# Optimization experiments

Hardware: AMD Instinct MI355X
Metric: run time of the kernel (lower is better)

Reference implementation:

```python
import jax, jax.numpy as jnp
import numpy as np

B, HG, WG = 2, 64, 64
N = HG * WG
C_IN, C_HID, HEADS, C_OUT = 512, 256, 4, 512
NEG_SLOPE = 0.2   # PyG GATv2Conv default negative_slope
LN_EPS = 1e-5


def _grid_edges(h, w):
    """8-neighborhood grid graph, edge_index[0]=source, edge_index[1]=target."""
    nodes = np.arange(h * w).reshape(h, w)
    srcs, dsts = [], []
    for dh in (-1, 0, 1):
        for dw in (-1, 0, 1):
            if dh == 0 and dw == 0:
                continue
            r0, r1 = max(0, -dh), h - max(0, dh)
            c0, c1 = max(0, -dw), w - max(0, dw)
            srcs.append(nodes[r0:r1, c0:c1].ravel())
            dsts.append(nodes[r0 + dh:r1 + dh, c0 + dw:c1 + dw].ravel())
    return np.stack([np.concatenate(srcs), np.concatenate(dsts)]).astype(np.int64)


def setup_inputs() -> dict:
    key = jax.random.key(0)
    ks = iter(jax.random.split(key, 32))

    def p(shape, scale=0.02):
        return jax.random.normal(next(ks), shape, dtype=jnp.float32) * scale

    return {
        "rgb_features": jax.random.normal(next(ks), (B, N, C_IN), dtype=jnp.float32),
        "x_features": jax.random.normal(next(ks), (B, N, C_IN), dtype=jnp.float32),
        "edge_index": jnp.asarray(_grid_edges(HG, WG)),
        # modality_fusion: Linear(2*C_IN, C_HID) + LayerNorm
        "fusion_w": p((C_HID, 2 * C_IN)), "fusion_b": jnp.zeros((C_HID,), jnp.float32),
        "fusion_g": jnp.ones((C_HID,), jnp.float32), "fusion_beta": jnp.zeros((C_HID,), jnp.float32),
        # GATSegmentation.in_proj + norm
        "inproj_w": p((C_HID, C_HID)), "inproj_b": jnp.zeros((C_HID,), jnp.float32),
        "norm_g": jnp.ones((C_HID,), jnp.float32), "norm_b": jnp.zeros((C_HID,), jnp.float32),
        # GATv2Conv layer 0: C_HID -> C_HID, heads=4, concat=True
        "l0_wl": p((HEADS * C_HID, C_HID)), "l0_bl": jnp.zeros((HEADS * C_HID,), jnp.float32),
        "l0_wr": p((HEADS * C_HID, C_HID)), "l0_br": jnp.zeros((HEADS * C_HID,), jnp.float32),
        "l0_att": p((HEADS, C_HID)), "l0_bias": jnp.zeros((HEADS * C_HID,), jnp.float32),
        # GATv2Conv layer 1 (final): 4*C_HID -> C_HID, heads=1, concat=False
        "l1_wl": p((C_HID, HEADS * C_HID)), "l1_bl": jnp.zeros((C_HID,), jnp.float32),
        "l1_wr": p((C_HID, HEADS * C_HID)), "l1_br": jnp.zeros((C_HID,), jnp.float32),
        "l1_att": p((1, C_HID)), "l1_bias": jnp.zeros((C_HID,), jnp.float32),
        # final_proj: 1x1 conv C_HID -> C_OUT
        "fp_w": p((C_OUT, C_HID)), "fp_b": jnp.zeros((C_OUT,), jnp.float32),
    }


def _ln(x, g, b):
    mu = x.mean(-1, keepdims=True)
    v = ((x - mu) ** 2).mean(-1, keepdims=True)
    return (x - mu) * jax.lax.rsqrt(v + LN_EPS) * g + b


def _gatv2(x, src, dst, wl, bl, wr, br, att, bias, concat):
    """PyG GATv2Conv (share_weights=False): gather, leaky_relu logit, segment softmax over
    target neighborhoods, scatter-add aggregation."""
    n = x.shape[0]
    heads, c = att.shape
    xl = (x @ wl.T + bl).reshape(n, heads, c)   # source-side transform (x_j)
    xr = (x @ wr.T + br).reshape(n, heads, c)   # target-side transform (x_i)
    e = jax.nn.leaky_relu(xl[src] + xr[dst], NEG_SLOPE)        # [E, H, C]
    logit = jnp.einsum('ehc,hc->eh', e, att)                   # [E, H]
    m = jax.ops.segment_max(logit, dst, num_segments=n)
    p = jnp.exp(logit - m[dst])
    z = jax.ops.segment_sum(p, dst, num_segments=n)
    alpha = p / z[dst]                                          # softmax per target node
    out = jax.ops.segment_sum(xl[src] * alpha[..., None], dst, num_segments=n)  # [N, H, C]
    out = out.reshape(n, heads * c) if concat else out.mean(axis=1)
    return out + bias


def reference(rgb_features, x_features, edge_index, fusion_w, fusion_b, fusion_g, fusion_beta,
              inproj_w, inproj_b, norm_g, norm_b,
              l0_wl, l0_bl, l0_wr, l0_br, l0_att, l0_bias,
              l1_wl, l1_bl, l1_wr, l1_br, l1_att, l1_bias,
              fp_w, fp_b):
    b, n, _ = rgb_features.shape
    loops = jnp.arange(n, dtype=edge_index.dtype)  # PyG add_self_loops=True
    src = jnp.concatenate([edge_index[0], loops])
    dst = jnp.concatenate([edge_index[1], loops])

    def single(rgb, xm):  # one graph in the batch (original loops over B in Python)
        comb = jnp.concatenate([rgb, xm], axis=-1)                     # [N, 2*C_IN]
        f = jax.nn.relu(_ln(comb @ fusion_w.T + fusion_b, fusion_g, fusion_beta))
        h = jax.nn.relu(_ln(f @ inproj_w.T + inproj_b, norm_g, norm_b))
        h = jax.nn.relu(_gatv2(h, src, dst, l0_wl, l0_bl, l0_wr, l0_br, l0_att, l0_bias, True))
        h = jax.nn.relu(_gatv2(h, src, dst, l1_wl, l1_bl, l1_wr, l1_br, l1_att, l1_bias, False))
        return h                                                        # [N, C_HID]

    nodes = jax.vmap(single)(rgb_features, x_features)                  # [B, N, C_HID]
    img = nodes.reshape(b, HG, WG, C_HID)
    return jnp.einsum('bhwc,oc->bohw', img, fp_w) + fp_b[None, :, None, None]
```

## Files before the change

### kernel.cpp

```cpp
#include <hip/hip_runtime.h>


#define NNODE 4096
#define LN_EPS 1e-5f
#define LOG2E 1.4426950408889634f

typedef _Float16 half8 __attribute__((ext_vector_type(8)));
typedef _Float16 half4 __attribute__((ext_vector_type(4)));
typedef _Float16 h2 __attribute__((ext_vector_type(2)));
typedef float f32x4 __attribute__((ext_vector_type(4)));

__device__ __forceinline__ float wave_reduce_sum(float v) {
    #pragma unroll
    for (int off = 32; off > 0; off >>= 1) v += __shfl_xor(v, off, 64);
    return v;
}

__device__ __forceinline__ void gload_lds16(const void* g, void* l) {
    __builtin_amdgcn_global_load_lds(
        (const __attribute__((address_space(1))) void*)g,
        (__attribute__((address_space(3))) void*)l, 16, 0, 0);
}

template<int N> __device__ __forceinline__ void waitcnt_vm() {
    if constexpr (N <= 0)      asm volatile("s_waitcnt vmcnt(0)" ::: "memory");
    else if constexpr (N == 2) asm volatile("s_waitcnt vmcnt(2)" ::: "memory");
    else if constexpr (N == 3) asm volatile("s_waitcnt vmcnt(3)" ::: "memory");
    else if constexpr (N == 4) asm volatile("s_waitcnt vmcnt(4)" ::: "memory");
    else                       asm volatile("s_waitcnt vmcnt(8)" ::: "memory");
}
__device__ __forceinline__ void barrier_raw() {
    asm volatile("s_barrier" ::: "memory");
}

__device__ __forceinline__ int xcd_swz(int lin, int total) {
    return (lin & 7) * (total >> 3) + (lin >> 3);
}

template<int IT, int JT, int OUTMODE>
__global__ __launch_bounds__(256) void gemm3_k(
    const _Float16* __restrict__ A, const _Float16* __restrict__ W,
    const float* __restrict__ bias_lo, const float* __restrict__ bias_hi,
    int nsplit, void* __restrict__ Cout, int K, int N)
{
    constexpr int BM = 32 * IT, BN = 32 * JT;
    constexpr int CA = (BM * 4) / 256;
    constexpr int CB = (BN * 4) / 256;
    constexpr int L = CA + CB;
    __shared__ _Float16 ldsA[3][BM * 32];
    __shared__ _Float16 ldsB[3][BN * 32];

    const int tid = threadIdx.x;
    const int lin = blockIdx.y * gridDim.x + blockIdx.x;
    const int swz = xcd_swz(lin, gridDim.x * gridDim.y);
    const int m0 = (swz / gridDim.x) * BM, n0 = (swz % gridDim.x) * BN;
    const int lane = tid & 63, w = tid >> 6;
    const int fr = lane & 15, kq = lane >> 4;
    const int sq = (kq ^ (fr & 3)) * 8;
    const int wm = (w & 1) * (16 * IT), wn = (w >> 1) * (16 * JT);

    const _Float16* aP[CA]; int aC[CA];
    #pragma unroll
    for (int i = 0; i < CA; ++i) {
        const int c = i * 256 + tid, r = c >> 2, q = (c & 3) ^ (r & 3);
        aP[i] = A + (size_t)(m0 + r) * K + q * 8;
        aC[i] = c * 8;
    }
    const _Float16* bP[CB]; int bC[CB];
    #pragma unroll
    for (int i = 0; i < CB; ++i) {
        const int c = i * 256 + tid, r = c >> 2, q = (c & 3) ^ (r & 3);
        bP[i] = W + (size_t)(n0 + r) * K + q * 8;
        bC[i] = c * 8;
    }

    f32x4 acc[IT][JT] = {};
    const int NT = K >> 5;

    #pragma unroll
    for (int i = 0; i < CA; ++i) gload_lds16(aP[i], &ldsA[0][aC[i]]);
    #pragma unroll
    for (int i = 0; i < CB; ++i) gload_lds16(bP[i], &ldsB[0][bC[i]]);
    #pragma unroll
    for (int i = 0; i < CA; ++i) gload_lds16(aP[i] + 32, &ldsA[1][aC[i]]);
    #pragma unroll
    for (int i = 0; i < CB; ++i) gload_lds16(bP[i] + 32, &ldsB[1][bC[i]]);

    int bi = 0;
    for (int t = 0; t < NT; ++t) {
        if (t + 1 < NT) waitcnt_vm<L>(); else waitcnt_vm<0>();
        barrier_raw();
        if (t + 2 < NT) {
            int nb = bi + 2; if (nb >= 3) nb -= 3;
            const int k2 = (t + 2) << 5;
            #pragma unroll
            for (int i = 0; i < CA; ++i) gload_lds16(aP[i] + k2, &ldsA[nb][aC[i]]);
            #pragma unroll
            for (int i = 0; i < CB; ++i) gload_lds16(bP[i] + k2, &ldsB[nb][bC[i]]);
        }
        half8 af[IT], bf[JT];
        #pragma unroll
        for (int i = 0; i < IT; ++i)
            af[i] = *(const half8*)&ldsA[bi][(wm + i * 16 + fr) * 32 + sq];
        #pragma unroll
        for (int j = 0; j < JT; ++j)
            bf[j] = *(const half8*)&ldsB[bi][(wn + j * 16 + fr) * 32 + sq];
        #pragma unroll
        for (int i = 0; i < IT; ++i)
            #pragma unroll
            for (int j = 0; j < JT; ++j) {
                if (OUTMODE == 1)
                    acc[i][j] = __builtin_amdgcn_mfma_f32_16x16x32_f16(
                        bf[j], af[i], acc[i][j], 0, 0, 0);
                else
                    acc[i][j] = __builtin_amdgcn_mfma_f32_16x16x32_f16(
                        af[i], bf[j], acc[i][j], 0, 0, 0);
            }
        ++bi; if (bi == 3) bi = 0;
    }

    if (OUTMODE == 1) {
        #pragma unroll
        for (int i = 0; i < IT; ++i) {
            const int m = m0 + wm + i * 16 + fr;
            #pragma unroll
            for (int j = 0; j < JT; ++j) {
                const int nb4 = n0 + wn + j * 16 + kq * 4;
                const float* bp = (nb4 < nsplit) ? bias_lo + nb4
                                                 : bias_hi + (nb4 - nsplit);
                const float4 bv = *(const float4*)bp;
                half4 ov = {(_Float16)(acc[i][j][0] + bv.x),
                            (_Float16)(acc[i][j][1] + bv.y),
                            (_Float16)(acc[i][j][2] + bv.z),
                            (_Float16)(acc[i][j][3] + bv.w)};
                *(half4*)((_Float16*)Cout + (size_t)m * N + nb4) = ov;
            }
        }
    } else {
        #pragma unroll
        for (int j = 0; j < JT; ++j) {
            const int col = n0 + wn + j * 16 + fr;
            const float bc = (col < nsplit) ? bias_lo[col] : bias_hi[col - nsplit];
            #pragma unroll
            for (int i = 0; i < IT; ++i) {
                const int mrun = m0 + wm + i * 16 + kq * 4;
                const int b = mrun >> 12, node = mrun & 4095;
                float4 ov = {acc[i][j][0] + bc, acc[i][j][1] + bc,
                             acc[i][j][2] + bc, acc[i][j][3] + bc};
                *(float4*)((float*)Cout + ((size_t)(b * N + col)) * 4096 + node) = ov;
            }
        }
    }
}

__global__ __launch_bounds__(512) void fusion2_k(
    const float* __restrict__ A0, const float* __restrict__ A1,
    const _Float16* __restrict__ W1, const float* __restrict__ b1,
    const float* __restrict__ g1, const float* __restrict__ be1,
    const _Float16* __restrict__ W2, const float* __restrict__ b2,
    const float* __restrict__ g2, const float* __restrict__ be2,
    _Float16* __restrict__ out)
{
    __shared__ _Float16 lA[2][16 * 32];
    __shared__ _Float16 lB[2][256 * 32];
    __shared__ float lC[16 * 260];
    __shared__ _Float16 lH[8 * 512];

    const int tid = threadIdx.x;
    const int m0 = blockIdx.x * 16;
    const int lane = tid & 63, w = tid >> 6;
    const int fr = lane & 15, kq = lane >> 4;
    const int sq = (kq ^ (fr & 3)) * 8;
    const int wc = w * 32;
    const bool stager = (tid < 64);

    const _Float16* bP[2]; int bC[2];
    #pragma unroll
    for (int i = 0; i < 2; ++i) {
        const int c = i * 512 + tid, r = c >> 2, q = (c & 3) ^ (r & 3);
        bP[i] = W1 + (size_t)r * 1024 + q * 8;
        bC[i] = c * 8;
    }
    const int ar = tid >> 2, aq = tid & 3;
    const int asw = (ar * 4 + (aq ^ (ar & 3))) * 8;
    float4 p0, p1;
    auto loadA = [&](int k) {
        const int gk = k + aq * 8;
        const float* s = (gk < 512) ? A0 + (size_t)(m0 + ar) * 512 + gk
                                    : A1 + (size_t)(m0 + ar) * 512 + gk - 512;
        p0 = *(const float4*)s;
        p1 = *(const float4*)(s + 4);
    };
    auto writeA = [&](int b) {
        half8 hv = {(_Float16)p0.x, (_Float16)p0.y, (_Float16)p0.z, (_Float16)p0.w,
                    (_Float16)p1.x, (_Float16)p1.y, (_Float16)p1.z, (_Float16)p1.w};
        *(half8*)&lA[b][asw] = hv;
    };

    f32x4 acc[2] = {};

    if (stager) { loadA(0); writeA(0); }
    #pragma unroll
    for (int i = 0; i < 2; ++i) gload_lds16(bP[i], &lB[0][bC[i]]);
    asm volatile("s_waitcnt vmcnt(0)" ::: "memory");
    __syncthreads();

    int cur = 0;
    for (int t = 0; t < 32; ++t) {
        const int pf = (t + 1 < 32);
        if (pf) {
            const int k1 = (t + 1) << 5;
            if (stager) loadA(k1);
            #pragma unroll
            for (int i = 0; i < 2; ++i) gload_lds16(bP[i] + k1, &lB[cur ^ 1][bC[i]]);
        }
        const half8 af = *(const half8*)&lA[cur][fr * 32 + sq];
        half8 bf[2];
        #pragma unroll
        for (int j = 0; j < 2; ++j)
            bf[j] = *(const half8*)&lB[cur][(wc + j * 16 + fr) * 32 + sq];
        #pragma unroll
        for (int j = 0; j < 2; ++j)
            acc[j] = __builtin_amdgcn_mfma_f32_16x16x32_f16(af, bf[j], acc[j], 0, 0, 0);
        if (pf) {
            if (stager) writeA(cur ^ 1);
            asm volatile("s_waitcnt vmcnt(0)" ::: "memory");
            __syncthreads();
            cur ^= 1;
        }
    }

    #pragma unroll
    for (int j = 0; j < 2; ++j) {
        const int col = wc + j * 16 + fr;
        const float bc = b1[col];
        #pragma unroll
        for (int r4 = 0; r4 < 4; ++r4)
            lC[(kq * 4 + r4) * 260 + col] = acc[j][r4] + bc;
    }
    __syncthreads();

    {
        const float4 gv = *(const float4*)(g1 + lane * 4);
        const float4 bv = *(const float4*)(be1 + lane * 4);
        const int t2i = lane >> 3, gq = (lane >> 1) & 3, qo = (lane & 1) * 4;
        #pragma unroll
        for (int rr = 0; rr < 2; ++rr) {
            const int row = w * 2 + rr;
            const float4 v = *(const float4*)&lC[row * 260 + lane * 4];
            float s  = v.x + v.y + v.z + v.w;
            float s2 = v.x * v.x + v.y * v.y + v.z * v.z + v.w * v.w;
            s = wave_reduce_sum(s);
            s2 = wave_reduce_sum(s2);
            const float mu  = s * (1.0f / 256.0f);
            const float var = s2 * (1.0f / 256.0f) - mu * mu;
            const float rs  = rsqrtf(var + LN_EPS);
            half4 o;
            o[0] = (_Float16)fmaxf((v.x - mu) * rs * gv.x + bv.x, 0.f);
            o[1] = (_Float16)fmaxf((v.y - mu) * rs * gv.y + bv.y, 0.f);
            o[2] = (_Float16)fmaxf((v.z - mu) * rs * gv.z + bv.z, 0.f);
            o[3] = (_Float16)fmaxf((v.w - mu) * rs * gv.w + bv.w, 0.f);
            const int qslot = gq ^ (row & 3);
            *(half4*)&lH[t2i * 512 + (row * 4 + qslot) * 8 + qo] = o;
        }
    }
    __syncthreads();

    const _Float16* b2P[2]; int b2C[2];
    #pragma unroll
    for (int i = 0; i < 2; ++i) {
        const int c = i * 512 + tid, r = c >> 2, q = (c & 3) ^ (r & 3);
        b2P[i] = W2 + (size_t)r * 256 + q * 8;
        b2C[i] = c * 8;
    }
    f32x4 acc2[2] = {};
    #pragma unroll
    for (int i = 0; i < 2; ++i) gload_lds16(b2P[i], &lB[0][b2C[i]]);
    asm volatile("s_waitcnt vmcnt(0)" ::: "memory");
    __syncthreads();

    int cur2 = 0;
    for (int t2 = 0; t2 < 8; ++t2) {
        const int pf = (t2 + 1 < 8);
        if (pf) {
            const int k1 = (t2 + 1) << 5;
            #pragma unroll
            for (int i = 0; i < 2; ++i) gload_lds16(b2P[i] + k1, &lB[cur2 ^ 1][b2C[i]]);
        }
        const half8 af = *(const half8*)
            &lH[t2 * 512 + (fr * 4 + (kq ^ (fr & 3))) * 8];
        half8 bf[2];
        #pragma unroll
        for (int j = 0; j < 2; ++j)
            bf[j] = *(const half8*)&lB[cur2][(wc + j * 16 + fr) * 32 + sq];
        #pragma unroll
        for (int j = 0; j < 2; ++j)
            acc2[j] = __builtin_amdgcn_mfma_f32_16x16x32_f16(af, bf[j], acc2[j], 0, 0, 0);
        if (pf) {
            asm volatile("s_waitcnt vmcnt(0)" ::: "memory");
            __syncthreads();
            cur2 ^= 1;
        }
    }

    __syncthreads();
    #pragma unroll
    for (int j = 0; j < 2; ++j) {
        const int col = wc + j * 16 + fr;
        const float bc = b2[col];
        #pragma unroll
        for (int r4 = 0; r4 < 4; ++r4)
            lC[(kq * 4 + r4) * 260 + col] = acc2[j][r4] + bc;
    }
    __syncthreads();

    {
        const float4 gv = *(const float4*)(g2 + lane * 4);
        const float4 bv = *(const float4*)(be2 + lane * 4);
        #pragma unroll
        for (int rr = 0; rr < 2; ++rr) {
            const int row = w * 2 + rr;
            const float4 v = *(const float4*)&lC[row * 260 + lane * 4];
            float s  = v.x + v.y + v.z + v.w;
            float s2 = v.x * v.x + v.y * v.y + v.z * v.z + v.w * v.w;
            s = wave_reduce_sum(s);
            s2 = wave_reduce_sum(s2);
            const float mu  = s * (1.0f / 256.0f);
            const float var = s2 * (1.0f / 256.0f) - mu * mu;
            const float rs  = rsqrtf(var + LN_EPS);
            half4 o;
            o[0] = (_Float16)fmaxf((v.x - mu) * rs * gv.x + bv.x, 0.f);
            o[1] = (_Float16)fmaxf((v.y - mu) * rs * gv.y + bv.y, 0.f);
            o[2] = (_Float16)fmaxf((v.z - mu) * rs * gv.z + bv.z, 0.f);
            o[3] = (_Float16)fmaxf((v.w - mu) * rs * gv.w + bv.w, 0.f);
            *(half4*)(out + (size_t)(m0 + row) * 256 + lane * 4) = o;
        }
    }
}

template<int HEADS, int LD, int XROFF, int OC>
__global__ __launch_bounds__(256) void gat4_k(
    const _Float16* __restrict__ xlr, const _Float16* __restrict__ att16,
    const float* __restrict__ bias, _Float16* __restrict__ out)
{
    const int tid = threadIdx.x, wv = tid >> 6, lane = tid & 63;
    const int g = lane >> 4, li = lane & 15;
    const int blk = xcd_swz(blockIdx.x, gridDim.x);
    const int wid = blk * 4 + wv;
    const int gi = (HEADS == 4) ? wid : wid * 4 + g;
    const int h  = (HEADS == 4) ? g : 0;
    const int node = gi & (NNODE - 1);
    const int base = gi - node;
    const int nr = node >> 6, nc = node & 63;
    const int co = h * 256 + li * 16;

    int sidx[9]; float msk[9];
    {
        const int drs[8] = {-1,-1,-1, 0, 0, 1, 1, 1};
        const int dcs[8] = {-1, 0, 1,-1, 1,-1, 0, 1};
        #pragma unroll
        for (int j = 0; j < 8; ++j) {
            const int rj = nr + drs[j], cj = nc + dcs[j];
            const bool v = ((unsigned)rj < 64u) & ((unsigned)cj < 64u);
            sidx[j] = v ? (rj * 64 + cj) : node;
            msk[j] = v ? 0.f : -1e30f;
        }
        sidx[8] = node; msk[8] = 0.f;
    }

    const _Float16* xp = xlr + (size_t)base * LD + co;

    half8 x0[9], x1[9];
    #pragma unroll
    for (int j = 0; j < 9; ++j) {
        x0[j] = *(const half8*)(xp + (size_t)sidx[j] * LD);
        x1[j] = *(const half8*)(xp + (size_t)sidx[j] * LD + 8);
    }
    const half8 xr0 = *(const half8*)(xlr + (size_t)gi * LD + XROFF + co);
    const half8 xr1 = *(const half8*)(xlr + (size_t)gi * LD + XROFF + co + 8);
    const half8 at0 = *(const half8*)(att16 + h * 256 + li * 16);
    const half8 at1 = *(const half8*)(att16 + h * 256 + li * 16 + 8);
    const h2 hz = {(_Float16)0.f, (_Float16)0.f};
    const h2 c02 = {(_Float16)0.2f, (_Float16)0.2f};

    float lg[9];
    #pragma unroll
    for (int j = 0; j < 9; ++j) {
        h2 p = hz;
        #pragma unroll
        for (int k = 0; k < 4; ++k) {
            h2 e = ((const h2*)&x0[j])[k] + ((const h2*)&xr0)[k];
            h2 tt = __builtin_elementwise_fma(
                __builtin_elementwise_min(e, hz), c02,
                __builtin_elementwise_max(e, hz));
            p = __builtin_elementwise_fma(tt, ((const h2*)&at0)[k], p);
        }
        #pragma unroll
        for (int k = 0; k < 4; ++k) {
            h2 e = ((const h2*)&x1[j])[k] + ((const h2*)&xr1)[k];
            h2 tt = __builtin_elementwise_fma(
                __builtin_elementwise_min(e, hz), c02,
                __builtin_elementwise_max(e, hz));
            p = __builtin_elementwise_fma(tt, ((const h2*)&at1)[k], p);
        }
        float pl = (float)p[0] + (float)p[1];
        pl += __shfl_xor(pl, 1, 64);
        pl += __shfl_xor(pl, 2, 64);
        pl += __shfl_xor(pl, 4, 64);
        pl += __shfl_xor(pl, 8, 64);
        lg[j] = pl + msk[j];
    }

    float m = lg[0];
    #pragma unroll
    for (int j = 1; j < 9; ++j) m = fmaxf(m, lg[j]);
    float pj[9], z = 0.f;
    #pragma unroll
    for (int j = 0; j < 9; ++j) { pj[j] = __builtin_amdgcn_exp2f(lg[j] - m); z += pj[j]; }
    const float inv = __builtin_amdgcn_rcpf(z);

    float acc[16];
    #pragma unroll
    for (int k = 0; k < 16; ++k) acc[k] = 0.f;
    #pragma unroll
    for (int j = 0; j < 9; ++j) {
        const float wj = pj[j];
        #pragma unroll
        for (int k = 0; k < 8; ++k) acc[k]     += wj * (float)x0[j][k];
        #pragma unroll
        for (int k = 0; k < 8; ++k) acc[8 + k] += wj * (float)x1[j][k];
    }
    float bv[16];
    #pragma unroll
    for (int q = 0; q < 4; ++q) {
        const float4 b4 = *(const float4*)(bias + h * 256 + li * 16 + q * 4);
        bv[q * 4 + 0] = b4.x; bv[q * 4 + 1] = b4.y;
        bv[q * 4 + 2] = b4.z; bv[q * 4 + 3] = b4.w;
    }
    half8 o0, o1;
    #pragma unroll
    for (int k = 0; k < 8; ++k) o0[k] = (_Float16)fmaxf(acc[k] * inv + bv[k], 0.f);
    #pragma unroll
    for (int k = 0; k < 8; ++k) o1[k] = (_Float16)fmaxf(acc[8 + k] * inv + bv[8 + k], 0.f);
    *(half8*)(out + (size_t)gi * OC + co) = o0;
    *(half8*)(out + (size_t)gi * OC + co + 8) = o1;
}

struct WTab {
    const float* src[9];
    int startblk[10];
    int nelem[9];
    int dstoff[9];
    float scale[9];
};

__global__ __launch_bounds__(256) void wconv_k(WTab t, _Float16* __restrict__ dst)
{
    const int b = blockIdx.x;
    int s = 0;
    #pragma unroll
    for (int i = 1; i < 9; ++i) s += (b >= t.startblk[i]);
    const int e0 = (b - t.startblk[s]) * 1024 + threadIdx.x * 4;
    if (e0 >= t.nelem[s]) return;
    const float4 v = *(const float4*)(t.src[s] + e0);
    const float sc = t.scale[s];
    half4 o = {(_Float16)(v.x * sc), (_Float16)(v.y * sc),
               (_Float16)(v.z * sc), (_Float16)(v.w * sc)};
    *(half4*)(dst + t.dstoff[s] + e0) = o;
}

extern "C" void kernel_launch(void* const* d_in, const int* in_sizes, int n_in,
                              void* d_out, int out_size, void* d_ws, size_t ws_size,
                              hipStream_t stream)
{
    const float* rgb       = (const float*)d_in[0];
    const float* xm        = (const float*)d_in[1];
    const float* fusion_w  = (const float*)d_in[3];
    const float* fusion_b  = (const float*)d_in[4];
    const float* fusion_g  = (const float*)d_in[5];
    const float* fusion_be = (const float*)d_in[6];
    const float* inproj_w  = (const float*)d_in[7];
    const float* inproj_b  = (const float*)d_in[8];
    const float* norm_g    = (const float*)d_in[9];
    const float* norm_b    = (const float*)d_in[10];
    const float* l0_wl     = (const float*)d_in[11];
    const float* l0_bl     = (const float*)d_in[12];
    const float* l0_wr     = (const float*)d_in[13];
    const float* l0_br     = (const float*)d_in[14];
    const float* l0_att    = (const float*)d_in[15];
    const float* l0_bias   = (const float*)d_in[16];
    const float* l1_wl     = (const float*)d_in[17];
    const float* l1_bl     = (const float*)d_in[18];
    const float* l1_wr     = (const float*)d_in[19];
    const float* l1_br     = (const float*)d_in[20];
    const float* l1_att    = (const float*)d_in[21];
    const float* l1_bias   = (const float*)d_in[22];
    const float* fp_w      = (const float*)d_in[23];
    const float* fp_b      = (const float*)d_in[24];

    char* ws = (char*)d_ws;
    _Float16* Wf16 = (_Float16*)ws;
    _Float16* H1   = (_Float16*)(ws + 4194304);
    _Float16* XLR0 = (_Float16*)(ws + 8388608);
    _Float16* GO0  = (_Float16*)(ws + 41943040);
    _Float16* XLR1 = (_Float16*)(ws + 58720256);
    _Float16* GO1  = (_Float16*)(ws + 67108864);

    _Float16* w_fus  = Wf16 + 0;
    _Float16* w_inp  = Wf16 + 262144;
    _Float16* w_l0   = Wf16 + 327680;
    _Float16* w_l1   = Wf16 + 851968;
    _Float16* w_fp   = Wf16 + 1376256;
    _Float16* att0_h = Wf16 + 1507328;
    _Float16* att1_h = Wf16 + 1508352;

    WTab t;
    const float* srcs[9] = {fusion_w, inproj_w, l0_wl, l0_wr, l1_wl, l1_wr,
                            fp_w, l0_att, l1_att};
    const int nel[9]  = {262144, 65536, 262144, 262144, 262144, 262144,
                         131072, 1024, 256};
    const int doff[9] = {0, 262144, 327680, 589824, 851968, 1114112,
                         1376256, 1507328, 1508352};
    const int sblk[10] = {0, 256, 320, 576, 832, 1088, 1344, 1472, 1473, 1474};
    for (int i = 0; i < 9; ++i) {
        t.src[i] = srcs[i]; t.nelem[i] = nel[i]; t.dstoff[i] = doff[i];
        t.scale[i] = (i >= 7) ? LOG2E : 1.0f;
    }
    for (int i = 0; i < 10; ++i) t.startblk[i] = sblk[i];

    wconv_k<<<1474, 256, 0, stream>>>(t, Wf16);

    fusion2_k<<<512, 512, 0, stream>>>(
        rgb, xm, w_fus, fusion_b, fusion_g, fusion_be,
        w_inp, inproj_b, norm_g, norm_b, H1);

    gemm3_k<4, 4, 1><<<dim3(16, 64), 256, 0, stream>>>(
        H1, w_l0, l0_bl, l0_br, 1024, XLR0, 256, 2048);

    gat4_k<4, 2048, 1024, 1024><<<2048, 256, 0, stream>>>(
        XLR0, att0_h, l0_bias, GO0);

    gemm3_k<2, 4, 1><<<dim3(4, 128), 256, 0, stream>>>(
        GO0, w_l1, l1_bl, l1_br, 256, XLR1, 1024, 512);

    gat4_k<1, 512, 256, 256><<<512, 256, 0, stream>>>(
        XLR1, att1_h, l1_bias, GO1);

    gemm3_k<2, 4, 2><<<dim3(4, 128), 256, 0, stream>>>(
        GO1, w_fp, fp_b, fp_b, 512, d_out, 256, 512);
}
```

Before: 117.4 us.

## Pre-convert fusion inputs to fp16 and triple-buffer fusion GEMM loads

The fp32 rgb and x inputs are now converted to fp16 and concatenated in a prep kernel that also converts the weights, replacing the separate weight-conversion launch. The fusion kernel can then stream A through async global-to-LDS loads like B. Both GEMM loops move from double to triple buffering, using partial vmcnt waits and a single barrier per step instead of full drains. This adds a full extra write and read of the converted activation buffer and more LDS per block, in exchange for better overlap of loads with MFMA work.

```diff
diff --git a/kernel.cpp b/kernel.cpp
--- a/kernel.cpp
+++ b/kernel.cpp
@@ -153,16 +153,16 @@
     }
 }
 
-__global__ __launch_bounds__(512) void fusion2_k(
-    const float* __restrict__ A0, const float* __restrict__ A1,
+__global__ __launch_bounds__(512) void fusion3_k(
+    const _Float16* __restrict__ Af,
     const _Float16* __restrict__ W1, const float* __restrict__ b1,
     const float* __restrict__ g1, const float* __restrict__ be1,
     const _Float16* __restrict__ W2, const float* __restrict__ b2,
     const float* __restrict__ g2, const float* __restrict__ be2,
     _Float16* __restrict__ out)
 {
-    __shared__ _Float16 lA[2][16 * 32];
-    __shared__ _Float16 lB[2][256 * 32];
+    __shared__ _Float16 lA[3][16 * 32];
+    __shared__ _Float16 lB[3][256 * 32];
     __shared__ float lC[16 * 260];
     __shared__ _Float16 lH[8 * 512];
 
@@ -181,53 +181,40 @@
         bP[i] = W1 + (size_t)r * 1024 + q * 8;
         bC[i] = c * 8;
     }
-    const int ar = tid >> 2, aq = tid & 3;
-    const int asw = (ar * 4 + (aq ^ (ar & 3))) * 8;
-    float4 p0, p1;
-    auto loadA = [&](int k) {
-        const int gk = k + aq * 8;
-        const float* s = (gk < 512) ? A0 + (size_t)(m0 + ar) * 512 + gk
-                                    : A1 + (size_t)(m0 + ar) * 512 + gk - 512;
-        p0 = *(const float4*)s;
-        p1 = *(const float4*)(s + 4);
-    };
-    auto writeA = [&](int b) {
-        half8 hv = {(_Float16)p0.x, (_Float16)p0.y, (_Float16)p0.z, (_Float16)p0.w,
-                    (_Float16)p1.x, (_Float16)p1.y, (_Float16)p1.z, (_Float16)p1.w};
-        *(half8*)&lA[b][asw] = hv;
-    };
+    const int arow = tid >> 2, aq = (tid & 3) ^ (arow & 3);
+    const _Float16* aP = Af + (size_t)(m0 + arow) * 1024 + aq * 8;
+    const int aC = tid * 8;
 
     f32x4 acc[2] = {};
 
-    if (stager) { loadA(0); writeA(0); }
+    if (stager) gload_lds16(aP, &lA[0][aC]);
     #pragma unroll
     for (int i = 0; i < 2; ++i) gload_lds16(bP[i], &lB[0][bC[i]]);
-    asm volatile("s_waitcnt vmcnt(0)" ::: "memory");
-    __syncthreads();
-
-    int cur = 0;
+    if (stager) gload_lds16(aP + 32, &lA[1][aC]);
+    #pragma unroll
+    for (int i = 0; i < 2; ++i) gload_lds16(bP[i] + 32, &lB[1][bC[i]]);
+
+    int bi = 0;
     for (int t = 0; t < 32; ++t) {
-        const int pf = (t + 1 < 32);
-        if (pf) {
-            const int k1 = (t + 1) << 5;
-            if (stager) loadA(k1);
-            #pragma unroll
-            for (int i = 0; i < 2; ++i) gload_lds16(bP[i] + k1, &lB[cur ^ 1][bC[i]]);
-        }
-        const half8 af = *(const half8*)&lA[cur][fr * 32 + sq];
+        if (t + 1 < 32) { if (stager) waitcnt_vm<3>(); else waitcnt_vm<2>(); }
+        else            waitcnt_vm<0>();
+        barrier_raw();
+        if (t + 2 < 32) {
+            int nb = bi + 2; if (nb >= 3) nb -= 3;
+            const int k2 = (t + 2) << 5;
+            if (stager) gload_lds16(aP + k2, &lA[nb][aC]);
+            #pragma unroll
+            for (int i = 0; i < 2; ++i) gload_lds16(bP[i] + k2, &lB[nb][bC[i]]);
+        }
+        const half8 af = *(const half8*)&lA[bi][fr * 32 + sq];
         half8 bf[2];
         #pragma unroll
         for (int j = 0; j < 2; ++j)
-            bf[j] = *(const half8*)&lB[cur][(wc + j * 16 + fr) * 32 + sq];
+            bf[j] = *(const half8*)&lB[bi][(wc + j * 16 + fr) * 32 + sq];
         #pragma unroll
         for (int j = 0; j < 2; ++j)
             acc[j] = __builtin_amdgcn_mfma_f32_16x16x32_f16(af, bf[j], acc[j], 0, 0, 0);
-        if (pf) {
-            if (stager) writeA(cur ^ 1);
-            asm volatile("s_waitcnt vmcnt(0)" ::: "memory");
-            __syncthreads();
-            cur ^= 1;
-        }
+        ++bi; if (bi == 3) bi = 0;
     }
 
     #pragma unroll
@@ -276,31 +263,29 @@
     f32x4 acc2[2] = {};
     #pragma unroll
     for (int i = 0; i < 2; ++i) gload_lds16(b2P[i], &lB[0][b2C[i]]);
-    asm volatile("s_waitcnt vmcnt(0)" ::: "memory");
-    __syncthreads();
-
-    int cur2 = 0;
+    #pragma unroll
+    for (int i = 0; i < 2; ++i) gload_lds16(b2P[i] + 32, &lB[1][b2C[i]]);
+
+    int bi2 = 0;
     for (int t2 = 0; t2 < 8; ++t2) {
-        const int pf = (t2 + 1 < 8);
-        if (pf) {
-            const int k1 = (t2 + 1) << 5;
-            #pragma unroll
-            for (int i = 0; i < 2; ++i) gload_lds16(b2P[i] + k1, &lB[cur2 ^ 1][b2C[i]]);
+        if (t2 + 1 < 8) waitcnt_vm<2>(); else waitcnt_vm<0>();
+        barrier_raw();
+        if (t2 + 2 < 8) {
+            int nb = bi2 + 2; if (nb >= 3) nb -= 3;
+            const int k2 = (t2 + 2) << 5;
+            #pragma unroll
+            for (int i = 0; i < 2; ++i) gload_lds16(b2P[i] + k2, &lB[nb][b2C[i]]);
         }
         const half8 af = *(const half8*)
             &lH[t2 * 512 + (fr * 4 + (kq ^ (fr & 3))) * 8];
         half8 bf[2];
         #pragma unroll
         for (int j = 0; j < 2; ++j)
-            bf[j] = *(const half8*)&lB[cur2][(wc + j * 16 + fr) * 32 + sq];
+            bf[j] = *(const half8*)&lB[bi2][(wc + j * 16 + fr) * 32 + sq];
         #pragma unroll
         for (int j = 0; j < 2; ++j)
             acc2[j] = __builtin_amdgcn_mfma_f32_16x16x32_f16(af, bf[j], acc2[j], 0, 0, 0);
-        if (pf) {
-            asm volatile("s_waitcnt vmcnt(0)" ::: "memory");
-            __syncthreads();
-            cur2 ^= 1;
-        }
+        ++bi2; if (bi2 == 3) bi2 = 0;
     }
 
     __syncthreads();
@@ -454,9 +439,24 @@
     float scale[9];
 };
 
-__global__ __launch_bounds__(256) void wconv_k(WTab t, _Float16* __restrict__ dst)
+__global__ __launch_bounds__(256) void prep_k(
+    const float* __restrict__ rgb, const float* __restrict__ xm,
+    _Float16* __restrict__ Cf16, WTab t, _Float16* __restrict__ dst)
 {
-    const int b = blockIdx.x;
+    if (blockIdx.x < 4096) {
+        const int idx = blockIdx.x * 256 + threadIdx.x;
+        const int m = idx >> 7;
+        const int k = (idx & 127) * 8;
+        const float* s = (k < 512) ? rgb + (size_t)m * 512 + k
+                                   : xm  + (size_t)m * 512 + (k - 512);
+        const float4 v0 = *(const float4*)s;
+        const float4 v1 = *(const float4*)(s + 4);
+        half8 o = {(_Float16)v0.x, (_Float16)v0.y, (_Float16)v0.z, (_Float16)v0.w,
+                   (_Float16)v1.x, (_Float16)v1.y, (_Float16)v1.z, (_Float16)v1.w};
+        *(half8*)(Cf16 + (size_t)m * 1024 + k) = o;
+        return;
+    }
+    const int b = blockIdx.x - 4096;
     int s = 0;
     #pragma unroll
     for (int i = 1; i < 9; ++i) s += (b >= t.startblk[i]);
@@ -505,6 +505,7 @@
     _Float16* GO0  = (_Float16*)(ws + 41943040);
     _Float16* XLR1 = (_Float16*)(ws + 58720256);
     _Float16* GO1  = (_Float16*)(ws + 67108864);
+    _Float16* Cf16 = (_Float16*)(ws + 71303168);
 
     _Float16* w_fus  = Wf16 + 0;
     _Float16* w_inp  = Wf16 + 262144;
@@ -528,10 +529,10 @@
     }
     for (int i = 0; i < 10; ++i) t.startblk[i] = sblk[i];
 
-    wconv_k<<<1474, 256, 0, stream>>>(t, Wf16);
-
-    fusion2_k<<<512, 512, 0, stream>>>(
-        rgb, xm, w_fus, fusion_b, fusion_g, fusion_be,
+    prep_k<<<4096 + 1474, 256, 0, stream>>>(rgb, xm, Cf16, t, Wf16);
+
+    fusion3_k<<<512, 512, 0, stream>>>(
+        Cf16, w_fus, fusion_b, fusion_g, fusion_be,
         w_inp, inproj_b, norm_g, norm_b, H1);
 
     gemm3_k<4, 4, 1><<<dim3(16, 64), 256, 0, stream>>>(
```

New measurement: 118.4 us, median of 2. About the same (+0.8%).
